# Kernel optimization log

Measured on AMD Instinct MI355X. Metric: run time of the kernel, lower is better.

Reference implementation:

```python
import jax, jax.numpy as jnp
import numpy as np

B, C, N = 8, 512, 2048
D = C // 8  # query/key dim


def setup_inputs() -> dict:
    key = jax.random.key(0)
    ks = jax.random.split(key, 6)
    x = jax.random.normal(ks[0], (B, C, N), dtype=jnp.float32)
    mask = jax.random.uniform(ks[1], (B, N), dtype=jnp.float32)
    Wq = jax.random.normal(ks[2], (D, C), dtype=jnp.float32) * (1.0 / np.sqrt(C))
    Wk = jax.random.normal(ks[3], (D, C), dtype=jnp.float32) * (1.0 / np.sqrt(C))
    Wv = jax.random.normal(ks[4], (C, C), dtype=jnp.float32) * (1.0 / np.sqrt(C))
    gamma = jax.random.normal(ks[5], (1,), dtype=jnp.float32)
    return {"x": x, "mask": mask, "Wq": Wq, "Wk": Wk, "Wv": Wv, "gamma": gamma}


def reference(x, mask, Wq, Wk, Wv, gamma):
    # 1x1 Conv1d (no bias) == channel matmul: (out,in) @ (B,in,N) -> (B,out,N)
    f = jnp.einsum('dc,bcn->bdn', Wq, x)   # query  (B, D, N)
    g = jnp.einsum('dc,bcn->bdn', Wk, x)   # key    (B, D, N)
    h = jnp.einsum('oc,bcn->bon', Wv, x)   # value  (B, C, N)
    # scores = f^T @ g : (B, N, N); act == identity ('none')
    scores = jnp.einsum('bdn,bdm->bnm', f, g)
    # column softmax: softmax over dim=1 (rows, i.e. first N axis)
    beta = jax.nn.softmax(scores, axis=1)  # (B, N, N)
    # post-softmax mask + renormalization over the same axis
    beta = beta * mask[:, :, None]
    beta = beta / (jnp.sum(beta, axis=1, keepdims=True) + 1e-12)
    # o = gamma * (h @ beta) + x
    o = gamma * jnp.einsum('bcn,bnm->bcm', h, beta) + x
    return o
```

## Files before the change

### kernel.cpp

```cpp
#include <hip/hip_runtime.h>
#include <hip/hip_bf16.h>

#define BB 8
#define CC 512
#define NN 2048
#define DD 64

typedef __attribute__((ext_vector_type(8))) _Float16 f16x8;
typedef __attribute__((ext_vector_type(4))) _Float16 f16x4;
typedef __attribute__((ext_vector_type(4))) float f32x4;

#define WS_XT  0u
#define WS_WF  16777216u
#define WS_FT  17432576u
#define WS_GT  19529728u
#define WS_H   21626880u
#define WS_M   38404096u
#define WS_IS  38469632u

#define HS0 0
#define HS1 65536
#define FS0 131072
#define FS1 139264
#define BTA 147456
#define LDS2B 155648

static __device__ __forceinline__ void gload_lds16(const void* g, void* l) {
    __builtin_amdgcn_global_load_lds(
        (const __attribute__((address_space(1))) void*)g,
        (__attribute__((address_space(3))) void*)l, 16, 0, 0);
}

static __device__ __forceinline__ void hard_barrier() {
    __builtin_amdgcn_sched_barrier(0);
    __builtin_amdgcn_s_barrier();
    __builtin_amdgcn_sched_barrier(0);
}

__global__ __launch_bounds__(256) void prep_kernel(
    const float* __restrict__ x, const float* __restrict__ Wq,
    const float* __restrict__ Wk, const float* __restrict__ Wv,
    _Float16* __restrict__ xT, _Float16* __restrict__ Wf)
{
    const int bid = blockIdx.x;
    const int t = threadIdx.x;
    if (bid >= 2048) {
        int e = ((bid - 2048) * 256 + t) * 8;
        const float* src;
        if (e < 32768) src = Wq + e;
        else if (e < 65536) src = Wk + (e - 32768);
        else src = Wv + (e - 65536);
        float4 v0 = *reinterpret_cast<const float4*>(src);
        float4 v1 = *reinterpret_cast<const float4*>(src + 4);
        f16x8 o = {(_Float16)v0.x, (_Float16)v0.y, (_Float16)v0.z, (_Float16)v0.w,
                   (_Float16)v1.x, (_Float16)v1.y, (_Float16)v1.z, (_Float16)v1.w};
        *reinterpret_cast<f16x8*>(Wf + e) = o;
        return;
    }
    __shared__ _Float16 xt[64][72];
    const int b = bid >> 8, ct = (bid >> 5) & 7, nt = bid & 31;
    const int cq = t & 15, nq = t >> 4;
    const float* xb = x + ((size_t)b * CC + 64 * ct + 4 * cq) * NN + 64 * nt + 4 * nq;
    float4 v0 = *reinterpret_cast<const float4*>(xb);
    float4 v1 = *reinterpret_cast<const float4*>(xb + NN);
    float4 v2 = *reinterpret_cast<const float4*>(xb + 2 * NN);
    float4 v3 = *reinterpret_cast<const float4*>(xb + 3 * NN);
    *reinterpret_cast<f16x4*>(&xt[4 * nq + 0][4 * cq]) =
        (f16x4){(_Float16)v0.x, (_Float16)v1.x, (_Float16)v2.x, (_Float16)v3.x};
    *reinterpret_cast<f16x4*>(&xt[4 * nq + 1][4 * cq]) =
        (f16x4){(_Float16)v0.y, (_Float16)v1.y, (_Float16)v2.y, (_Float16)v3.y};
    *reinterpret_cast<f16x4*>(&xt[4 * nq + 2][4 * cq]) =
        (f16x4){(_Float16)v0.z, (_Float16)v1.z, (_Float16)v2.z, (_Float16)v3.z};
    *reinterpret_cast<f16x4*>(&xt[4 * nq + 3][4 * cq]) =
        (f16x4){(_Float16)v0.w, (_Float16)v1.w, (_Float16)v2.w, (_Float16)v3.w};
    __syncthreads();
    #pragma unroll
    for (int rr = 0; rr < 2; rr++) {
        int nl = (t >> 3) + 32 * rr, c8 = t & 7;
        f16x8 vv = *reinterpret_cast<const f16x8*>(&xt[nl][8 * c8]);
        *reinterpret_cast<f16x8*>(&xT[((size_t)b * NN + 64 * nt + nl) * CC + 64 * ct + 8 * c8]) = vv;
    }
}

__global__ __launch_bounds__(512) void proj_kernel(
    const _Float16* __restrict__ xT, const _Float16* __restrict__ Wf,
    const float* __restrict__ mask,
    _Float16* __restrict__ fT, _Float16* __restrict__ gT, _Float16* __restrict__ h)
{
    const int nb = blockIdx.x, b = blockIdx.y;
    const int n0 = nb * 64;
    const int t = threadIdx.x, w = t >> 6, l = t & 63, lo = l & 15, hi = l >> 4;
    const _Float16* xTb = xT + ((size_t)b * NN + n0) * CC;

    f32x4 acc[5][4];
    #pragma unroll
    for (int i = 0; i < 5; i++)
        #pragma unroll
        for (int j = 0; j < 4; j++) acc[i][j] = (f32x4){0.f, 0.f, 0.f, 0.f};

    #pragma unroll 2
    for (int ks = 0; ks < 16; ks++) {
        f16x8 bfr[4];
        #pragma unroll
        for (int nf = 0; nf < 4; nf++)
            bfr[nf] = *reinterpret_cast<const f16x8*>(xTb + (size_t)(16 * nf + lo) * CC + 32 * ks + 8 * hi);
        #pragma unroll
        for (int rf = 0; rf < 5; rf++) {
            f16x8 af = *reinterpret_cast<const f16x8*>(
                Wf + (size_t)(16 * (w + 8 * rf) + lo) * CC + 32 * ks + 8 * hi);
            #pragma unroll
            for (int nf = 0; nf < 4; nf++)
                acc[rf][nf] = __builtin_amdgcn_mfma_f32_16x16x32_f16(af, bfr[nf], acc[rf][nf], 0, 0, 0);
        }
    }

    float mask4[4];
    #pragma unroll
    for (int nf = 0; nf < 4; nf++) mask4[nf] = mask[(size_t)b * NN + n0 + 16 * nf + lo];

    #pragma unroll
    for (int rf = 0; rf < 5; rf++) {
        int Rb = 16 * (w + 8 * rf);
        #pragma unroll
        for (int nf = 0; nf < 4; nf++) {
            int n = n0 + 16 * nf + lo;
            if (Rb < 64) {
                f16x4 v = {(_Float16)acc[rf][nf][0], (_Float16)acc[rf][nf][1],
                           (_Float16)acc[rf][nf][2], (_Float16)acc[rf][nf][3]};
                *reinterpret_cast<f16x4*>(&fT[((size_t)b * NN + n) * DD + Rb + 4 * hi]) = v;
            } else if (Rb < 128) {
                f16x4 v = {(_Float16)acc[rf][nf][0], (_Float16)acc[rf][nf][1],
                           (_Float16)acc[rf][nf][2], (_Float16)acc[rf][nf][3]};
                *reinterpret_cast<f16x4*>(&gT[((size_t)b * NN + n) * DD + (Rb - 64) + 4 * hi]) = v;
            } else {
                int cr = Rb - 128 + 4 * hi;
                #pragma unroll
                for (int j = 0; j < 4; j++)
                    h[((size_t)b * CC + cr + j) * NN + n] = (_Float16)(acc[rf][nf][j] * mask4[nf]);
            }
        }
    }
}

__global__ __launch_bounds__(512) void stats_kernel(
    const _Float16* __restrict__ fT, const _Float16* __restrict__ gT,
    const float* __restrict__ mask, float* __restrict__ Mg, float* __restrict__ iSg)
{
    const int bid = blockIdx.x;
    const int b = bid & 7, mb = bid >> 3;
    const int m0 = mb * 64;
    const int t = threadIdx.x, w = t >> 6, l = t & 63, lo = l & 15, hi = l >> 4;

    __shared__ float masks_all[NN];
    __shared__ float sm[8][64], ss[8][64];

    *reinterpret_cast<float4*>(&masks_all[t * 4]) =
        *reinterpret_cast<const float4*>(&mask[(size_t)b * NN + t * 4]);
    __syncthreads();

    const _Float16* gTb = gT + (size_t)b * NN * DD;
    const _Float16* fTb = fT + (size_t)b * NN * DD;

    f16x8 bq[4][2];
    #pragma unroll
    for (int mf = 0; mf < 4; mf++)
        #pragma unroll
        for (int kk = 0; kk < 2; kk++)
            bq[mf][kk] = *reinterpret_cast<const f16x8*>(
                gTb + (size_t)(m0 + 16 * mf + lo) * DD + 32 * kk + 8 * hi);

    float m_run[4] = {-1e30f, -1e30f, -1e30f, -1e30f};
    float s_run[4] = {0.f, 0.f, 0.f, 0.f};

    for (int tl = 0; tl < 4; tl++) {
        const int nbase = (w + 8 * tl) * 64;
        f16x8 afr[4][2];
        #pragma unroll
        for (int rf = 0; rf < 4; rf++)
            #pragma unroll
            for (int kk = 0; kk < 2; kk++)
                afr[rf][kk] = *reinterpret_cast<const f16x8*>(
                    fTb + (size_t)(nbase + 16 * rf + lo) * DD + 32 * kk + 8 * hi);
        f32x4 s[4][4];
        #pragma unroll
        for (int rf = 0; rf < 4; rf++)
            #pragma unroll
            for (int mf = 0; mf < 4; mf++) {
                f32x4 a4 = (f32x4){0.f, 0.f, 0.f, 0.f};
                a4 = __builtin_amdgcn_mfma_f32_16x16x32_f16(afr[rf][0], bq[mf][0], a4, 0, 0, 0);
                a4 = __builtin_amdgcn_mfma_f32_16x16x32_f16(afr[rf][1], bq[mf][1], a4, 0, 0, 0);
                s[rf][mf] = a4;
            }
        #pragma unroll
        for (int mf = 0; mf < 4; mf++) {
            float mx = -1e30f;
            #pragma unroll
            for (int rf = 0; rf < 4; rf++)
                #pragma unroll
                for (int j = 0; j < 4; j++) mx = fmaxf(mx, s[rf][mf][j]);
            float nm = fmaxf(m_run[mf], mx);
            float sum = 0.f;
            #pragma unroll
            for (int rf = 0; rf < 4; rf++)
                #pragma unroll
                for (int j = 0; j < 4; j++)
                    sum += masks_all[nbase + 16 * rf + 4 * hi + j] * __expf(s[rf][mf][j] - nm);
            s_run[mf] = s_run[mf] * __expf(m_run[mf] - nm) + sum;
            m_run[mf] = nm;
        }
    }
    #pragma unroll
    for (int mf = 0; mf < 4; mf++) {
        #pragma unroll
        for (int d = 16; d <= 32; d <<= 1) {
            float om = __shfl_xor(m_run[mf], d);
            float os = __shfl_xor(s_run[mf], d);
            float nm = fmaxf(m_run[mf], om);
            s_run[mf] = s_run[mf] * __expf(m_run[mf] - nm) + os * __expf(om - nm);
            m_run[mf] = nm;
        }
    }
    if (l < 16) {
        #pragma unroll
        for (int mf = 0; mf < 4; mf++) { sm[w][16 * mf + l] = m_run[mf]; ss[w][16 * mf + l] = s_run[mf]; }
    }
    __syncthreads();
    if (t < 64) {
        float M = -1e30f;
        #pragma unroll
        for (int w8 = 0; w8 < 8; w8++) M = fmaxf(M, sm[w8][t]);
        float S = 0.f;
        #pragma unroll
        for (int w8 = 0; w8 < 8; w8++) S += ss[w8][t] * __expf(sm[w8][t] - M);
        Mg[(size_t)b * NN + m0 + t] = M;
        iSg[(size_t)b * NN + m0 + t] = 1.0f / (S + 1e-20f);
    }
}

__global__ __launch_bounds__(512) void attn2_kernel(
    const _Float16* __restrict__ fT, const _Float16* __restrict__ gT,
    const _Float16* __restrict__ h, const float* __restrict__ x,
    const float* __restrict__ Mg, const float* __restrict__ iSg,
    const float* __restrict__ gamma, float* __restrict__ out)
{
    extern __shared__ __align__(16) char smem[];
    const int bid = blockIdx.x;
    const int b = bid & 7, mb = bid >> 3;
    const int m0 = mb * 64;
    const int t = threadIdx.x, w = t >> 6, l = t & 63, lo = l & 15, hi = l >> 4;
    const int wn = w & 3, wm = w >> 2;
    const int r3 = l >> 3, c3 = l & 7;
    const int sch = c3 ^ r3;

    const _Float16* hb = h + (size_t)b * CC * NN;
    const _Float16* fTb = fT + (size_t)b * NN * DD;

    f16x8 bq[2][2]; float Mr[2], iSr[2];
    #pragma unroll
    for (int mf = 0; mf < 2; mf++) {
        int m = m0 + 32 * wm + 16 * mf + lo;
        #pragma unroll
        for (int kk = 0; kk < 2; kk++)
            bq[mf][kk] = *reinterpret_cast<const f16x8*>(
                gT + ((size_t)b * NN + m) * DD + 32 * kk + 8 * hi);
        Mr[mf] = Mg[(size_t)b * NN + m];
        iSr[mf] = iSg[(size_t)b * NN + m];
    }

    f32x4 o[4][4];
    #pragma unroll
    for (int ci = 0; ci < 4; ci++)
        #pragma unroll
        for (int mi = 0; mi < 4; mi++) o[ci][mi] = (f32x4){0.f, 0.f, 0.f, 0.f};

    #define STAGE(ti, bs) do {                                                         \
        int _n0 = (ti) * 64;                                                           \
        char* _hd = smem + ((bs) ? HS1 : HS0) + (64 * w) * 128;                        \
        const _Float16* _hs = hb + (size_t)(64 * w + r3) * NN + _n0 + sch * 8;         \
        _Pragma("unroll")                                                              \
        for (int _r = 0; _r < 8; _r++)                                                 \
            gload_lds16((const void*)(_hs + (size_t)(8 * _r) * NN), (void*)(_hd + _r * 1024)); \
        char* _fd = smem + ((bs) ? FS1 : FS0) + (8 * w) * 128;                         \
        const _Float16* _fs = fTb + (size_t)(_n0 + 8 * w + r3) * DD + sch * 8;         \
        gload_lds16((const void*)_fs, (void*)_fd);                                     \
    } while (0)

    STAGE(0, 0);

    #pragma unroll 1
    for (int i = 0; i < 32; i++) {
        const int cur = i & 1;
        if (i < 31) {
            STAGE(i + 1, cur ^ 1);
            asm volatile("s_waitcnt vmcnt(9)" ::: "memory");
        } else {
            asm volatile("s_waitcnt vmcnt(0)" ::: "memory");
        }
        hard_barrier();

        char* fsb = smem + (cur ? FS1 : FS0);
        const int arow = 16 * wn + lo;
        f16x8 af0 = *reinterpret_cast<const f16x8*>(fsb + arow * 128 + ((hi ^ (lo & 7)) * 16));
        f16x8 af1 = *reinterpret_cast<const f16x8*>(fsb + arow * 128 + (((4 + hi) ^ (lo & 7)) * 16));
        f32x4 s[2];
        #pragma unroll
        for (int mf = 0; mf < 2; mf++) {
            f32x4 a4 = (f32x4){0.f, 0.f, 0.f, 0.f};
            a4 = __builtin_amdgcn_mfma_f32_16x16x32_f16(af0, bq[mf][0], a4, 0, 0, 0);
            a4 = __builtin_amdgcn_mfma_f32_16x16x32_f16(af1, bq[mf][1], a4, 0, 0, 0);
            s[mf] = a4;
        }

        char* btb = smem + BTA;
        #pragma unroll
        for (int mf = 0; mf < 2; mf++) {
            f16x4 ev;
            #pragma unroll
            for (int j = 0; j < 4; j++)
                ev[j] = (_Float16)(__expf(s[mf][j] - Mr[mf]) * iSr[mf]);
            int m = 32 * wm + 16 * mf + lo;
            int chunk = (2 * wn + (hi >> 1)) ^ (lo & 7);
            *reinterpret_cast<f16x4*>(btb + m * 128 + chunk * 16 + (hi & 1) * 8) = ev;
        }
        asm volatile("s_waitcnt lgkmcnt(0)" ::: "memory");
        hard_barrier();

        char* hsb = smem + (cur ? HS1 : HS0);
        #pragma unroll
        for (int kk = 0; kk < 2; kk++) {
            f16x8 bb[4];
            #pragma unroll
            for (int mi = 0; mi < 4; mi++)
                bb[mi] = *reinterpret_cast<const f16x8*>(
                    btb + (16 * mi + lo) * 128 + (((4 * kk + hi) ^ (lo & 7)) * 16));
            #pragma unroll
            for (int ci = 0; ci < 4; ci++) {
                f16x8 ah = *reinterpret_cast<const f16x8*>(
                    hsb + (64 * w + 16 * ci + lo) * 128 + (((4 * kk + hi) ^ (lo & 7)) * 16));
                #pragma unroll
                for (int mi = 0; mi < 4; mi++)
                    o[ci][mi] = __builtin_amdgcn_mfma_f32_16x16x32_f16(ah, bb[mi], o[ci][mi], 0, 0, 0);
            }
        }
        asm volatile("s_waitcnt lgkmcnt(0)" ::: "memory");
        hard_barrier();
    }
    #undef STAGE

    char* ob = smem + w * 17408;
    #pragma unroll
    for (int ci = 0; ci < 4; ci++)
        #pragma unroll
        for (int mi = 0; mi < 4; mi++)
            #pragma unroll
            for (int j = 0; j < 4; j++)
                *reinterpret_cast<float*>(ob + (16 * ci + 4 * hi + j) * 272 + (16 * mi + lo) * 4) =
                    o[ci][mi][j];

    const float gm = gamma[0];
    const float* xb = x + (size_t)b * CC * NN;
    float* outb = out + (size_t)b * CC * NN;
    #pragma unroll
    for (int rr = 0; rr < 16; rr++) {
        int row = 4 * rr + hi;
        int mq = lo;
        f32x4 v = *reinterpret_cast<const f32x4*>(ob + row * 272 + mq * 16);
        size_t idx = (size_t)(64 * w + row) * NN + m0 + mq * 4;
        float4 xv = *reinterpret_cast<const float4*>(xb + idx);
        float4 res;
        res.x = gm * v[0] + xv.x; res.y = gm * v[1] + xv.y;
        res.z = gm * v[2] + xv.z; res.w = gm * v[3] + xv.w;
        *reinterpret_cast<float4*>(outb + idx) = res;
    }
}

extern "C" void kernel_launch(void* const* d_in, const int* in_sizes, int n_in,
                              void* d_out, int out_size, void* d_ws, size_t ws_size,
                              hipStream_t stream) {
    (void)in_sizes; (void)n_in; (void)out_size; (void)ws_size;
    const float* x     = (const float*)d_in[0];
    const float* mask  = (const float*)d_in[1];
    const float* Wq    = (const float*)d_in[2];
    const float* Wk    = (const float*)d_in[3];
    const float* Wv    = (const float*)d_in[4];
    const float* gamma = (const float*)d_in[5];
    float* out = (float*)d_out;

    char* ws = (char*)d_ws;
    _Float16* xT = (_Float16*)(ws + WS_XT);
    _Float16* Wf = (_Float16*)(ws + WS_WF);
    _Float16* fT = (_Float16*)(ws + WS_FT);
    _Float16* gT = (_Float16*)(ws + WS_GT);
    _Float16* h  = (_Float16*)(ws + WS_H);
    float* Mg  = (float*)(ws + WS_M);
    float* iSg = (float*)(ws + WS_IS);

    prep_kernel<<<2208, 256, 0, stream>>>(x, Wq, Wk, Wv, xT, Wf);
    proj_kernel<<<dim3(32, 8), 512, 0, stream>>>(xT, Wf, mask, fT, gT, h);
    stats_kernel<<<256, 512, 0, stream>>>(fT, gT, mask, Mg, iSg);
    hipFuncSetAttribute((const void*)attn2_kernel,
                        hipFuncAttributeMaxDynamicSharedMemorySize, LDS2B);
    attn2_kernel<<<256, 512, LDS2B, stream>>>(fT, gT, h, x, Mg, iSg, gamma, out);
}
```

Measured before the change: 206.2 us.

## Fuse x transpose into projection, split stats over N, retile attention kernel

Drops the separate x-to-fp16 transpose pass: the projection kernel now loads fp32 x directly, converts it and stores it transposed into swizzled LDS. The stats kernel splits the softmax N range into two halves across twice as many blocks, writing partial max and sum values that the attention kernel merges. The attention kernel is retiled to 128 output columns by 256 channels per block. It double-buffers the probability tile and replaces the prefetch-then-partial-wait pattern with a full wait and one barrier per iteration. The epilogue goes through a smaller swizzled LDS staging area, which cuts LDS use and removes the xT round trip through global memory, at the cost of less load/compute overlap in the main loop.

```diff
diff --git a/kernel.cpp b/kernel.cpp
--- a/kernel.cpp
+++ b/kernel.cpp
@@ -10,20 +10,17 @@
 typedef __attribute__((ext_vector_type(4))) _Float16 f16x4;
 typedef __attribute__((ext_vector_type(4))) float f32x4;
 
-#define WS_XT  0u
-#define WS_WF  16777216u
-#define WS_FT  17432576u
-#define WS_GT  19529728u
-#define WS_H   21626880u
-#define WS_M   38404096u
-#define WS_IS  38469632u
+#define WS_WF 0u
+#define WS_FT 1048576u
+#define WS_GT 3145728u
+#define WS_H  5242880u
+#define WS_M  22020096u
+#define WS_S  22151168u
 
 #define HS0 0
-#define HS1 65536
-#define FS0 131072
-#define FS1 139264
-#define BTA 147456
-#define LDS2B 155648
+#define FS0 65536
+#define BT0 81920
+#define LDS2B 114688
 
 static __device__ __forceinline__ void gload_lds16(const void* g, void* l) {
     __builtin_amdgcn_global_load_lds(
@@ -37,60 +34,50 @@
     __builtin_amdgcn_sched_barrier(0);
 }
 
-__global__ __launch_bounds__(256) void prep_kernel(
-    const float* __restrict__ x, const float* __restrict__ Wq,
-    const float* __restrict__ Wk, const float* __restrict__ Wv,
-    _Float16* __restrict__ xT, _Float16* __restrict__ Wf)
+__global__ __launch_bounds__(256) void wconv_kernel(
+    const float* __restrict__ Wq, const float* __restrict__ Wk,
+    const float* __restrict__ Wv, _Float16* __restrict__ Wf)
 {
-    const int bid = blockIdx.x;
-    const int t = threadIdx.x;
-    if (bid >= 2048) {
-        int e = ((bid - 2048) * 256 + t) * 8;
-        const float* src;
-        if (e < 32768) src = Wq + e;
-        else if (e < 65536) src = Wk + (e - 32768);
-        else src = Wv + (e - 65536);
-        float4 v0 = *reinterpret_cast<const float4*>(src);
-        float4 v1 = *reinterpret_cast<const float4*>(src + 4);
-        f16x8 o = {(_Float16)v0.x, (_Float16)v0.y, (_Float16)v0.z, (_Float16)v0.w,
-                   (_Float16)v1.x, (_Float16)v1.y, (_Float16)v1.z, (_Float16)v1.w};
-        *reinterpret_cast<f16x8*>(Wf + e) = o;
-        return;
-    }
-    __shared__ _Float16 xt[64][72];
-    const int b = bid >> 8, ct = (bid >> 5) & 7, nt = bid & 31;
-    const int cq = t & 15, nq = t >> 4;
-    const float* xb = x + ((size_t)b * CC + 64 * ct + 4 * cq) * NN + 64 * nt + 4 * nq;
-    float4 v0 = *reinterpret_cast<const float4*>(xb);
-    float4 v1 = *reinterpret_cast<const float4*>(xb + NN);
-    float4 v2 = *reinterpret_cast<const float4*>(xb + 2 * NN);
-    float4 v3 = *reinterpret_cast<const float4*>(xb + 3 * NN);
-    *reinterpret_cast<f16x4*>(&xt[4 * nq + 0][4 * cq]) =
-        (f16x4){(_Float16)v0.x, (_Float16)v1.x, (_Float16)v2.x, (_Float16)v3.x};
-    *reinterpret_cast<f16x4*>(&xt[4 * nq + 1][4 * cq]) =
-        (f16x4){(_Float16)v0.y, (_Float16)v1.y, (_Float16)v2.y, (_Float16)v3.y};
-    *reinterpret_cast<f16x4*>(&xt[4 * nq + 2][4 * cq]) =
-        (f16x4){(_Float16)v0.z, (_Float16)v1.z, (_Float16)v2.z, (_Float16)v3.z};
-    *reinterpret_cast<f16x4*>(&xt[4 * nq + 3][4 * cq]) =
-        (f16x4){(_Float16)v0.w, (_Float16)v1.w, (_Float16)v2.w, (_Float16)v3.w};
-    __syncthreads();
-    #pragma unroll
-    for (int rr = 0; rr < 2; rr++) {
-        int nl = (t >> 3) + 32 * rr, c8 = t & 7;
-        f16x8 vv = *reinterpret_cast<const f16x8*>(&xt[nl][8 * c8]);
-        *reinterpret_cast<f16x8*>(&xT[((size_t)b * NN + 64 * nt + nl) * CC + 64 * ct + 8 * c8]) = vv;
-    }
-}
-
-__global__ __launch_bounds__(512) void proj_kernel(
-    const _Float16* __restrict__ xT, const _Float16* __restrict__ Wf,
+    int e = (blockIdx.x * 256 + threadIdx.x) * 8;
+    const float* src;
+    if (e < 32768) src = Wq + e;
+    else if (e < 65536) src = Wk + (e - 32768);
+    else src = Wv + (e - 65536);
+    float4 v0 = *reinterpret_cast<const float4*>(src);
+    float4 v1 = *reinterpret_cast<const float4*>(src + 4);
+    f16x8 o = {(_Float16)v0.x, (_Float16)v0.y, (_Float16)v0.z, (_Float16)v0.w,
+               (_Float16)v1.x, (_Float16)v1.y, (_Float16)v1.z, (_Float16)v1.w};
+    *reinterpret_cast<f16x8*>(Wf + e) = o;
+}
+
+__global__ __launch_bounds__(512, 2) void proj_kernel(
+    const float* __restrict__ x, const _Float16* __restrict__ Wf,
     const float* __restrict__ mask,
     _Float16* __restrict__ fT, _Float16* __restrict__ gT, _Float16* __restrict__ h)
 {
     const int nb = blockIdx.x, b = blockIdx.y;
     const int n0 = nb * 64;
     const int t = threadIdx.x, w = t >> 6, l = t & 63, lo = l & 15, hi = l >> 4;
-    const _Float16* xTb = xT + ((size_t)b * NN + n0) * CC;
+
+    __shared__ _Float16 xs[64][512];
+
+    const float* xb = x + (size_t)b * CC * NN + n0;
+    {
+        const int cq = t >> 4, nq = t & 15;
+        #pragma unroll 4
+        for (int p = 0; p < 16; p++) {
+            int c = 32 * p + cq;
+            float4 v = *reinterpret_cast<const float4*>(xb + (size_t)c * NN + 4 * nq);
+            int cc = c >> 3, cb = c & 7;
+            float vv[4] = {v.x, v.y, v.z, v.w};
+            #pragma unroll
+            for (int j = 0; j < 4; j++) {
+                int n = 4 * nq + j;
+                xs[n][(((cc ^ (n & 7)) << 3) | cb)] = (_Float16)vv[j];
+            }
+        }
+    }
+    __syncthreads();
 
     f32x4 acc[5][4];
     #pragma unroll
@@ -98,12 +85,13 @@
         #pragma unroll
         for (int j = 0; j < 4; j++) acc[i][j] = (f32x4){0.f, 0.f, 0.f, 0.f};
 
-    #pragma unroll 2
+    #pragma unroll 4
     for (int ks = 0; ks < 16; ks++) {
         f16x8 bfr[4];
         #pragma unroll
         for (int nf = 0; nf < 4; nf++)
-            bfr[nf] = *reinterpret_cast<const f16x8*>(xTb + (size_t)(16 * nf + lo) * CC + 32 * ks + 8 * hi);
+            bfr[nf] = *reinterpret_cast<const f16x8*>(
+                &xs[16 * nf + lo][((4 * ks + hi) ^ (lo & 7)) << 3]);
         #pragma unroll
         for (int rf = 0; rf < 5; rf++) {
             f16x8 af = *reinterpret_cast<const f16x8*>(
@@ -142,24 +130,24 @@
     }
 }
 
-__global__ __launch_bounds__(512) void stats_kernel(
+__global__ __launch_bounds__(512, 2) void stats_kernel(
     const _Float16* __restrict__ fT, const _Float16* __restrict__ gT,
-    const float* __restrict__ mask, float* __restrict__ Mg, float* __restrict__ iSg)
+    const float* __restrict__ mask, float* __restrict__ Mp, float* __restrict__ Sp)
 {
     const int bid = blockIdx.x;
-    const int b = bid & 7, mb = bid >> 3;
+    const int b = bid & 7, mb = (bid >> 3) & 31, ns = bid >> 8;
     const int m0 = mb * 64;
     const int t = threadIdx.x, w = t >> 6, l = t & 63, lo = l & 15, hi = l >> 4;
 
-    __shared__ float masks_all[NN];
+    __shared__ float masks_l[1024];
     __shared__ float sm[8][64], ss[8][64];
 
-    *reinterpret_cast<float4*>(&masks_all[t * 4]) =
-        *reinterpret_cast<const float4*>(&mask[(size_t)b * NN + t * 4]);
+    *reinterpret_cast<float2*>(&masks_l[2 * t]) =
+        *reinterpret_cast<const float2*>(&mask[(size_t)b * NN + ns * 1024 + 2 * t]);
     __syncthreads();
 
     const _Float16* gTb = gT + (size_t)b * NN * DD;
-    const _Float16* fTb = fT + (size_t)b * NN * DD;
+    const _Float16* fTb = fT + ((size_t)b * NN + ns * 1024) * DD;
 
     f16x8 bq[4][2];
     #pragma unroll
@@ -172,39 +160,38 @@
     float m_run[4] = {-1e30f, -1e30f, -1e30f, -1e30f};
     float s_run[4] = {0.f, 0.f, 0.f, 0.f};
 
-    for (int tl = 0; tl < 4; tl++) {
-        const int nbase = (w + 8 * tl) * 64;
+    #pragma unroll
+    for (int tl = 0; tl < 2; tl++) {
+        const int nl = (w + 8 * tl) * 64;
         f16x8 afr[4][2];
         #pragma unroll
         for (int rf = 0; rf < 4; rf++)
             #pragma unroll
             for (int kk = 0; kk < 2; kk++)
                 afr[rf][kk] = *reinterpret_cast<const f16x8*>(
-                    fTb + (size_t)(nbase + 16 * rf + lo) * DD + 32 * kk + 8 * hi);
-        f32x4 s[4][4];
-        #pragma unroll
-        for (int rf = 0; rf < 4; rf++)
-            #pragma unroll
-            for (int mf = 0; mf < 4; mf++) {
+                    fTb + (size_t)(nl + 16 * rf + lo) * DD + 32 * kk + 8 * hi);
+        #pragma unroll
+        for (int mf = 0; mf < 4; mf++) {
+            f32x4 s4[4];
+            #pragma unroll
+            for (int rf = 0; rf < 4; rf++) {
                 f32x4 a4 = (f32x4){0.f, 0.f, 0.f, 0.f};
                 a4 = __builtin_amdgcn_mfma_f32_16x16x32_f16(afr[rf][0], bq[mf][0], a4, 0, 0, 0);
                 a4 = __builtin_amdgcn_mfma_f32_16x16x32_f16(afr[rf][1], bq[mf][1], a4, 0, 0, 0);
-                s[rf][mf] = a4;
-            }
-        #pragma unroll
-        for (int mf = 0; mf < 4; mf++) {
+                s4[rf] = a4;
+            }
             float mx = -1e30f;
             #pragma unroll
             for (int rf = 0; rf < 4; rf++)
                 #pragma unroll
-                for (int j = 0; j < 4; j++) mx = fmaxf(mx, s[rf][mf][j]);
+                for (int j = 0; j < 4; j++) mx = fmaxf(mx, s4[rf][j]);
             float nm = fmaxf(m_run[mf], mx);
             float sum = 0.f;
             #pragma unroll
             for (int rf = 0; rf < 4; rf++)
                 #pragma unroll
                 for (int j = 0; j < 4; j++)
-                    sum += masks_all[nbase + 16 * rf + 4 * hi + j] * __expf(s[rf][mf][j] - nm);
+                    sum += masks_l[nl + 16 * rf + 4 * hi + j] * __expf(s4[rf][j] - nm);
             s_run[mf] = s_run[mf] * __expf(m_run[mf] - nm) + sum;
             m_run[mf] = nm;
         }
@@ -232,25 +219,25 @@
         float S = 0.f;
         #pragma unroll
         for (int w8 = 0; w8 < 8; w8++) S += ss[w8][t] * __expf(sm[w8][t] - M);
-        Mg[(size_t)b * NN + m0 + t] = M;
-        iSg[(size_t)b * NN + m0 + t] = 1.0f / (S + 1e-20f);
-    }
-}
-
-__global__ __launch_bounds__(512) void attn2_kernel(
+        Mp[(size_t)(ns * 8 + b) * NN + m0 + t] = M;
+        Sp[(size_t)(ns * 8 + b) * NN + m0 + t] = S;
+    }
+}
+
+__global__ __launch_bounds__(512, 1) void attn2_kernel(
     const _Float16* __restrict__ fT, const _Float16* __restrict__ gT,
     const _Float16* __restrict__ h, const float* __restrict__ x,
-    const float* __restrict__ Mg, const float* __restrict__ iSg,
+    const float* __restrict__ Mp, const float* __restrict__ Sp,
     const float* __restrict__ gamma, float* __restrict__ out)
 {
     extern __shared__ __align__(16) char smem[];
     const int bid = blockIdx.x;
-    const int b = bid & 7, mb = bid >> 3;
-    const int m0 = mb * 64;
+    const int b = bid & 7, mb2 = (bid >> 3) & 15, cs2 = bid >> 7;
+    const int m0 = mb2 * 128, cbase = cs2 * 256;
     const int t = threadIdx.x, w = t >> 6, l = t & 63, lo = l & 15, hi = l >> 4;
-    const int wn = w & 3, wm = w >> 2;
-    const int r3 = l >> 3, c3 = l & 7;
-    const int sch = c3 ^ r3;
+    const int r3 = l >> 3, c3 = l & 7, sch = c3 ^ r3;
+    const int sn = 32 * (w & 1), smg = 32 * (w >> 1);
+    const int cg = w & 3, mg = w >> 2;
 
     const _Float16* hb = h + (size_t)b * CC * NN;
     const _Float16* fTb = fT + (size_t)b * NN * DD;
@@ -258,13 +245,16 @@
     f16x8 bq[2][2]; float Mr[2], iSr[2];
     #pragma unroll
     for (int mf = 0; mf < 2; mf++) {
-        int m = m0 + 32 * wm + 16 * mf + lo;
+        int m = m0 + smg + 16 * mf + lo;
         #pragma unroll
         for (int kk = 0; kk < 2; kk++)
             bq[mf][kk] = *reinterpret_cast<const f16x8*>(
                 gT + ((size_t)b * NN + m) * DD + 32 * kk + 8 * hi);
-        Mr[mf] = Mg[(size_t)b * NN + m];
-        iSr[mf] = iSg[(size_t)b * NN + m];
+        float M0 = Mp[(size_t)b * NN + m],       S0 = Sp[(size_t)b * NN + m];
+        float M1 = Mp[(size_t)(8 + b) * NN + m], S1 = Sp[(size_t)(8 + b) * NN + m];
+        float M = fmaxf(M0, M1);
+        float S = S0 * __expf(M0 - M) + S1 * __expf(M1 - M);
+        Mr[mf] = M; iSr[mf] = 1.0f / (S + 1e-20f);
     }
 
     f32x4 o[4][4];
@@ -274,13 +264,13 @@
         for (int mi = 0; mi < 4; mi++) o[ci][mi] = (f32x4){0.f, 0.f, 0.f, 0.f};
 
     #define STAGE(ti, bs) do {                                                         \
-        int _n0 = (ti) * 64;                                                           \
-        char* _hd = smem + ((bs) ? HS1 : HS0) + (64 * w) * 128;                        \
-        const _Float16* _hs = hb + (size_t)(64 * w + r3) * NN + _n0 + sch * 8;         \
+        const int _n0 = (ti) * 64;                                                     \
+        char* _hd = smem + (bs) * 32768 + (32 * w) * 128;                              \
+        const _Float16* _hs = hb + (size_t)(cbase + 32 * w + r3) * NN + _n0 + sch * 8; \
         _Pragma("unroll")                                                              \
-        for (int _r = 0; _r < 8; _r++)                                                 \
-            gload_lds16((const void*)(_hs + (size_t)(8 * _r) * NN), (void*)(_hd + _r * 1024)); \
-        char* _fd = smem + ((bs) ? FS1 : FS0) + (8 * w) * 128;                         \
+        for (int _q = 0; _q < 4; _q++)                                                 \
+            gload_lds16((const void*)(_hs + (size_t)(8 * _q) * NN), (void*)(_hd + _q * 1024)); \
+        char* _fd = smem + FS0 + (bs) * 8192 + (8 * w) * 128;                          \
         const _Float16* _fs = fTb + (size_t)(_n0 + 8 * w + r3) * DD + sch * 8;         \
         gload_lds16((const void*)_fs, (void*)_fd);                                     \
     } while (0)
@@ -290,87 +280,102 @@
     #pragma unroll 1
     for (int i = 0; i < 32; i++) {
         const int cur = i & 1;
-        if (i < 31) {
-            STAGE(i + 1, cur ^ 1);
-            asm volatile("s_waitcnt vmcnt(9)" ::: "memory");
-        } else {
-            asm volatile("s_waitcnt vmcnt(0)" ::: "memory");
-        }
+        asm volatile("s_waitcnt vmcnt(0)" ::: "memory");
         hard_barrier();
-
-        char* fsb = smem + (cur ? FS1 : FS0);
-        const int arow = 16 * wn + lo;
-        f16x8 af0 = *reinterpret_cast<const f16x8*>(fsb + arow * 128 + ((hi ^ (lo & 7)) * 16));
-        f16x8 af1 = *reinterpret_cast<const f16x8*>(fsb + arow * 128 + (((4 + hi) ^ (lo & 7)) * 16));
-        f32x4 s[2];
-        #pragma unroll
-        for (int mf = 0; mf < 2; mf++) {
-            f32x4 a4 = (f32x4){0.f, 0.f, 0.f, 0.f};
-            a4 = __builtin_amdgcn_mfma_f32_16x16x32_f16(af0, bq[mf][0], a4, 0, 0, 0);
-            a4 = __builtin_amdgcn_mfma_f32_16x16x32_f16(af1, bq[mf][1], a4, 0, 0, 0);
-            s[mf] = a4;
-        }
-
-        char* btb = smem + BTA;
-        #pragma unroll
-        for (int mf = 0; mf < 2; mf++) {
-            f16x4 ev;
-            #pragma unroll
-            for (int j = 0; j < 4; j++)
-                ev[j] = (_Float16)(__expf(s[mf][j] - Mr[mf]) * iSr[mf]);
-            int m = 32 * wm + 16 * mf + lo;
-            int chunk = (2 * wn + (hi >> 1)) ^ (lo & 7);
-            *reinterpret_cast<f16x4*>(btb + m * 128 + chunk * 16 + (hi & 1) * 8) = ev;
-        }
+        if (i < 31) STAGE(i + 1, cur ^ 1);
+
+        char* fsb = smem + FS0 + cur * 8192;
+        char* btb = smem + BT0 + cur * 16384;
+        f32x4 s4[2][2];
+        #pragma unroll
+        for (int rf = 0; rf < 2; rf++)
+            #pragma unroll
+            for (int mf = 0; mf < 2; mf++) s4[rf][mf] = (f32x4){0.f, 0.f, 0.f, 0.f};
+        #pragma unroll
+        for (int rf = 0; rf < 2; rf++) {
+            int nrow = sn + 16 * rf + lo;
+            #pragma unroll
+            for (int kk = 0; kk < 2; kk++) {
+                f16x8 af = *reinterpret_cast<const f16x8*>(
+                    fsb + nrow * 128 + (((4 * kk + hi) ^ (lo & 7)) << 4));
+                #pragma unroll
+                for (int mf = 0; mf < 2; mf++)
+                    s4[rf][mf] = __builtin_amdgcn_mfma_f32_16x16x32_f16(af, bq[mf][kk], s4[rf][mf], 0, 0, 0);
+            }
+        }
+        #pragma unroll
+        for (int rf = 0; rf < 2; rf++)
+            #pragma unroll
+            for (int mf = 0; mf < 2; mf++) {
+                f16x4 ev;
+                #pragma unroll
+                for (int j = 0; j < 4; j++)
+                    ev[j] = (_Float16)(__expf(s4[rf][mf][j] - Mr[mf]) * iSr[mf]);
+                int ml = smg + 16 * mf + lo;
+                int nl = sn + 16 * rf + 4 * hi;
+                int chunk = (nl >> 3) ^ (lo & 7);
+                *reinterpret_cast<f16x4*>(btb + ml * 128 + chunk * 16 + (nl & 7) * 2) = ev;
+            }
         asm volatile("s_waitcnt lgkmcnt(0)" ::: "memory");
         hard_barrier();
 
-        char* hsb = smem + (cur ? HS1 : HS0);
+        char* hsb = smem + cur * 32768;
         #pragma unroll
         for (int kk = 0; kk < 2; kk++) {
             f16x8 bb[4];
             #pragma unroll
-            for (int mi = 0; mi < 4; mi++)
+            for (int mi = 0; mi < 4; mi++) {
+                int ml = 64 * mg + 16 * mi + lo;
                 bb[mi] = *reinterpret_cast<const f16x8*>(
-                    btb + (16 * mi + lo) * 128 + (((4 * kk + hi) ^ (lo & 7)) * 16));
+                    btb + ml * 128 + (((4 * kk + hi) ^ (lo & 7)) << 4));
+            }
             #pragma unroll
             for (int ci = 0; ci < 4; ci++) {
+                int crow = 64 * cg + 16 * ci + lo;
                 f16x8 ah = *reinterpret_cast<const f16x8*>(
-                    hsb + (64 * w + 16 * ci + lo) * 128 + (((4 * kk + hi) ^ (lo & 7)) * 16));
+                    hsb + crow * 128 + (((4 * kk + hi) ^ (lo & 7)) << 4));
                 #pragma unroll
                 for (int mi = 0; mi < 4; mi++)
                     o[ci][mi] = __builtin_amdgcn_mfma_f32_16x16x32_f16(ah, bb[mi], o[ci][mi], 0, 0, 0);
             }
         }
-        asm volatile("s_waitcnt lgkmcnt(0)" ::: "memory");
-        hard_barrier();
     }
     #undef STAGE
 
-    char* ob = smem + w * 17408;
-    #pragma unroll
-    for (int ci = 0; ci < 4; ci++)
-        #pragma unroll
-        for (int mi = 0; mi < 4; mi++)
-            #pragma unroll
-            for (int j = 0; j < 4; j++)
-                *reinterpret_cast<float*>(ob + (16 * ci + 4 * hi + j) * 272 + (16 * mi + lo) * 4) =
-                    o[ci][mi][j];
-
+    __syncthreads();
+
+    float* ob = reinterpret_cast<float*>(smem + w * 9216);
     const float gm = gamma[0];
     const float* xb = x + (size_t)b * CC * NN;
     float* outb = out + (size_t)b * CC * NN;
-    #pragma unroll
-    for (int rr = 0; rr < 16; rr++) {
-        int row = 4 * rr + hi;
-        int mq = lo;
-        f32x4 v = *reinterpret_cast<const f32x4*>(ob + row * 272 + mq * 16);
-        size_t idx = (size_t)(64 * w + row) * NN + m0 + mq * 4;
-        float4 xv = *reinterpret_cast<const float4*>(xb + idx);
-        float4 res;
-        res.x = gm * v[0] + xv.x; res.y = gm * v[1] + xv.y;
-        res.z = gm * v[2] + xv.z; res.w = gm * v[3] + xv.w;
-        *reinterpret_cast<float4*>(outb + idx) = res;
+
+    #pragma unroll
+    for (int half = 0; half < 2; half++) {
+        #pragma unroll
+        for (int ci = 0; ci < 4; ci++)
+            #pragma unroll
+            for (int mh = 0; mh < 2; mh++) {
+                int mi = 2 * half + mh;
+                #pragma unroll
+                for (int j = 0; j < 4; j++) {
+                    int row = 16 * ci + 4 * hi + j;
+                    int ml = 16 * mh + lo;
+                    ob[row * 36 + (((ml >> 2) ^ (row & 7)) << 2) + (ml & 3)] = o[ci][mi][j];
+                }
+            }
+        asm volatile("s_waitcnt lgkmcnt(0)" ::: "memory");
+        #pragma unroll
+        for (int rr = 0; rr < 8; rr++) {
+            int row = 8 * rr + r3;
+            f32x4 v = *reinterpret_cast<const f32x4*>(ob + row * 36 + ((c3 ^ (row & 7)) << 2));
+            size_t idx = (size_t)(cbase + 64 * cg + row) * NN + m0 + 64 * mg + 32 * half + 4 * c3;
+            float4 xv = *reinterpret_cast<const float4*>(xb + idx);
+            float4 res;
+            res.x = gm * v[0] + xv.x; res.y = gm * v[1] + xv.y;
+            res.z = gm * v[2] + xv.z; res.w = gm * v[3] + xv.w;
+            *reinterpret_cast<float4*>(outb + idx) = res;
+        }
+        asm volatile("s_waitcnt lgkmcnt(0)" ::: "memory");
     }
 }
 
@@ -387,18 +392,17 @@
     float* out = (float*)d_out;
 
     char* ws = (char*)d_ws;
-    _Float16* xT = (_Float16*)(ws + WS_XT);
     _Float16* Wf = (_Float16*)(ws + WS_WF);
     _Float16* fT = (_Float16*)(ws + WS_FT);
     _Float16* gT = (_Float16*)(ws + WS_GT);
     _Float16* h  = (_Float16*)(ws + WS_H);
-    float* Mg  = (float*)(ws + WS_M);
-    float* iSg = (float*)(ws + WS_IS);
-
-    prep_kernel<<<2208, 256, 0, stream>>>(x, Wq, Wk, Wv, xT, Wf);
-    proj_kernel<<<dim3(32, 8), 512, 0, stream>>>(xT, Wf, mask, fT, gT, h);
-    stats_kernel<<<256, 512, 0, stream>>>(fT, gT, mask, Mg, iSg);
+    float* Mp = (float*)(ws + WS_M);
+    float* Sp = (float*)(ws + WS_S);
+
+    wconv_kernel<<<160, 256, 0, stream>>>(Wq, Wk, Wv, Wf);
+    proj_kernel<<<dim3(32, 8), 512, 0, stream>>>(x, Wf, mask, fT, gT, h);
+    stats_kernel<<<512, 512, 0, stream>>>(fT, gT, mask, Mp, Sp);
     hipFuncSetAttribute((const void*)attn2_kernel,
                         hipFuncAttributeMaxDynamicSharedMemorySize, LDS2B);
-    attn2_kernel<<<256, 512, LDS2B, stream>>>(fT, gT, h, x, Mg, iSg, gamma, out);
-}
+    attn2_kernel<<<256, 512, LDS2B, stream>>>(fT, gT, h, x, Mp, Sp, gamma, out);
+}
```

After: 188.1 us. 8.8% less time.
